# Kernel optimization log

Hardware: AMD Instinct MI355X
Metric: run time of the kernel (lower is better)

Reference implementation:

```python
import jax, jax.numpy as jnp
import numpy as np

B, H, W = 16, 1024, 1024
EPS = 1e-7
FG_PROB = 0.1  # foreground pixel probability for synthetic gt


def setup_inputs() -> dict:
    key = jax.random.key(0)
    k1, k2 = jax.random.split(key)
    probs = jax.random.normal(k1, (B, 2, H, W), dtype=jnp.float32)
    gt = (jax.random.uniform(k2, (B, H, W)) < FG_PROB).astype(jnp.float32)
    gt_f_num = gt.sum(axis=(1, 2))  # per-sample foreground pixel count (float)
    return {"probs": probs, "gt": gt, "gt_f_num": gt_f_num, "img_h": H, "img_w": W}


def reference(probs, gt, gt_f_num, img_h, img_w):
    # foreground probability, clamped
    pc = jax.nn.softmax(probs, axis=1)[:, 1, :, :]
    pc = jnp.clip(pc, EPS, 1.0 - EPS)
    b = pc.shape[0]
    f_loss = -(gt * jnp.log(pc)).reshape(b, -1)          # [B, N]
    b_loss = -((1.0 - gt) * jnp.log(1.0 - pc)).reshape(b, -1)  # [B, N]
    n = b_loss.shape[1]

    # sort background loss descending per sample; top gt_f_num[i] entries are
    # "difficult" negatives, the rest are "simple" (equivalent to the torch
    # gather-into-zero-buffers since only sums/counts are taken afterwards)
    sorted_b = -jnp.sort(-b_loss, axis=1)                # descending, [B, N]
    k = gt_f_num.astype(jnp.int32)                       # int(gt_f_num[i])
    mask = jnp.arange(n, dtype=jnp.int32)[None, :] < k[:, None]  # [B, N]

    difficult_sum = jnp.sum(jnp.where(mask, sorted_b, 0.0), axis=1)
    simple_sum = jnp.sum(jnp.where(mask, 0.0, sorted_b), axis=1)
    difficult_num = jnp.sum(mask & (sorted_b != 0.0), axis=1).astype(jnp.float32)

    difficult_b_loss = difficult_sum / (difficult_num + 1e-16)
    simple_b_loss = simple_sum / (float(img_h * img_w) + 1e-16)
    f_loss_mean = f_loss.sum(axis=1) / (gt_f_num + 1e-16)

    return difficult_b_loss.mean() + f_loss_mean.mean() + simple_b_loss.mean()
```

## Files before the change

kernel.cpp:

```cpp
#include <hip/hip_runtime.h>
#include <math.h>

#define NB 16
#define NPIX 1048576
#define BINS 4096
#define CHUNKS 64
#define TPB_A 512
#define PIX_PER_BLOCK (NPIX / CHUNKS)
#define PPT 8
#define ITERS_A (PIX_PER_BLOCK / (TPB_A * PPT))
#define TPB_B 256
#define BINS_PER_CHUNK (BINS / TPB_B)
#define BLOSS_MAX 16.2f
#define BINW (BLOSS_MAX / (float)BINS)
#define B_CAP 15.9424f
#define F_CAP 16.1181f

__device__ __forceinline__ void fadd_glb(float* p, float v) {
    __hip_atomic_fetch_add(p, v, __ATOMIC_RELAXED, __HIP_MEMORY_SCOPE_AGENT);
}

__global__ __launch_bounds__(TPB_A) void pass_a(
    const float* __restrict__ probs, const float* __restrict__ gt,
    unsigned* __restrict__ g_cnt, float* __restrict__ f_sum,
    float* __restrict__ b_sum)
{
    __shared__ unsigned s_cnt[BINS];
    __shared__ float s_redf[TPB_A / 64];
    __shared__ float s_redb[TPB_A / 64];

    const int tid = threadIdx.x;
    for (int j = tid; j < BINS; j += TPB_A) s_cnt[j] = 0u;
    __syncthreads();

    const int blk = blockIdx.x;
    const int b = blk / CHUNKS;
    const int chunk = blk % CHUNKS;
    const float* p0 = probs + (size_t)b * 2 * NPIX;
    const float* p1 = p0 + NPIX;
    const float* gp = gt + (size_t)b * NPIX;
    const int base = chunk * PIX_PER_BLOCK;
    const float scale = (float)BINS / BLOSS_MAX;

    float f_acc = 0.f, b_acc = 0.f;

    float4 cA0, cB0, cA1, cB1, cG0, cG1;
    {
        const int i = base + (tid << 2);
        const int i2 = i + TPB_A * 4;
        cA0 = *(const float4*)(p0 + i);  cB0 = *(const float4*)(p0 + i2);
        cA1 = *(const float4*)(p1 + i);  cB1 = *(const float4*)(p1 + i2);
        cG0 = *(const float4*)(gp + i);  cG1 = *(const float4*)(gp + i2);
    }
    for (int it = 0; it < ITERS_A; ++it) {
        float4 nA0, nB0, nA1, nB1, nG0, nG1;
        {
            const int nit = (it + 1 < ITERS_A) ? it + 1 : it;
            const int i = base + nit * (TPB_A * PPT) + (tid << 2);
            const int i2 = i + TPB_A * 4;
            nA0 = *(const float4*)(p0 + i);  nB0 = *(const float4*)(p0 + i2);
            nA1 = *(const float4*)(p1 + i);  nB1 = *(const float4*)(p1 + i2);
            nG0 = *(const float4*)(gp + i);  nG1 = *(const float4*)(gp + i2);
        }
        const float dv[PPT] = {cA1.x - cA0.x, cA1.y - cA0.y, cA1.z - cA0.z, cA1.w - cA0.w,
                               cB1.x - cB0.x, cB1.y - cB0.y, cB1.z - cB0.z, cB1.w - cB0.w};
        const float gv[PPT] = {cG0.x, cG0.y, cG0.z, cG0.w, cG1.x, cG1.y, cG1.z, cG1.w};
        #pragma unroll
        for (int q = 0; q < PPT; ++q) {
            const float d = dv[q];
            const float sp = fmaxf(d, 0.f) + __logf(1.f + __expf(-fabsf(d)));
            if (gv[q] > 0.5f) {
                f_acc += fminf(sp - d, F_CAP);
            } else {
                const float bl = fminf(sp, B_CAP);
                b_acc += bl;
                int bin = (int)(bl * scale);
                bin = bin < (BINS - 1) ? bin : (BINS - 1);
                atomicAdd(&s_cnt[bin], 1u);
            }
        }
        cA0 = nA0; cB0 = nB0; cA1 = nA1; cB1 = nB1; cG0 = nG0; cG1 = nG1;
    }
    __syncthreads();

    for (int j = tid; j < BINS; j += TPB_A) {
        const unsigned c = s_cnt[j];
        if (c) atomicAdd(&g_cnt[(size_t)b * BINS + j], c);
    }

    #pragma unroll
    for (int o = 32; o > 0; o >>= 1) {
        f_acc += __shfl_down(f_acc, o, 64);
        b_acc += __shfl_down(b_acc, o, 64);
    }
    if ((tid & 63) == 0) { s_redf[tid >> 6] = f_acc; s_redb[tid >> 6] = b_acc; }
    __syncthreads();
    if (tid == 0) {
        float f = 0.f, bs = 0.f;
        #pragma unroll
        for (int w = 0; w < TPB_A / 64; ++w) { f += s_redf[w]; bs += s_redb[w]; }
        fadd_glb(&f_sum[b], f);
        fadd_glb(&b_sum[b], bs);
    }
}

__global__ __launch_bounds__(TPB_B) void pass_b(
    const unsigned* __restrict__ g_cnt, const float* __restrict__ f_sum,
    const float* __restrict__ b_sum, const float* __restrict__ gt_f_num,
    float* __restrict__ terms)
{
    __shared__ unsigned s_cnt[BINS];
    __shared__ unsigned s_suf[TPB_B];
    __shared__ double s_wsuf[TPB_B];
    __shared__ double s_dsum;

    const int b = blockIdx.x;
    const int t = threadIdx.x;

    for (int j = 0; j < BINS_PER_CHUNK; ++j) {
        const int bin = j * TPB_B + t;
        s_cnt[bin] = g_cnt[(size_t)b * BINS + bin];
    }
    __syncthreads();

    unsigned c = 0; double w = 0.0;
    const int cb = t * BINS_PER_CHUNK;
    for (int j = 0; j < BINS_PER_CHUNK; ++j) {
        const unsigned cc = s_cnt[cb + j];
        c += cc;
        w += (double)cc * (double)(((float)(cb + j) + 0.5f) * BINW);
    }
    s_suf[t] = c; s_wsuf[t] = w;
    __syncthreads();

    for (int off = 1; off < TPB_B; off <<= 1) {
        const unsigned ac = (t + off < TPB_B) ? s_suf[t + off] : 0u;
        const double aw = (t + off < TPB_B) ? s_wsuf[t + off] : 0.0;
        __syncthreads();
        s_suf[t] += ac; s_wsuf[t] += aw;
        __syncthreads();
    }

    const long long kk = (long long)gt_f_num[b];
    const unsigned long long n_pos = (unsigned long long)s_suf[0];
    const unsigned long long suf_me = s_suf[t];
    const unsigned long long suf_nx = (t + 1 < TPB_B) ? s_suf[t + 1] : 0ull;

    if (kk > 0 && (unsigned long long)kk < n_pos &&
        suf_nx < (unsigned long long)kk && (unsigned long long)kk <= suf_me) {
        unsigned long long cum = suf_nx;
        double W = (t + 1 < TPB_B) ? s_wsuf[t + 1] : 0.0;
        int bstar = cb;
        for (int j = BINS_PER_CHUNK - 1; j >= 0; --j) {
            const int bin = cb + j;
            const unsigned cc = s_cnt[bin];
            if (cum + cc >= (unsigned long long)kk) { bstar = bin; break; }
            cum += cc;
            W += (double)cc * (double)(((float)bin + 0.5f) * BINW);
        }
        const double partial = (double)(kk - (long long)cum);
        s_dsum = W + partial * (double)(((float)bstar + 0.5f) * BINW);
    }
    __syncthreads();

    if (t == 0) {
        const double S_total = (double)b_sum[b];
        const double fs = (double)f_sum[b];
        const double gfn = (double)gt_f_num[b];
        double dsum, dnum;
        if (kk <= 0) { dsum = 0.0; dnum = 0.0; }
        else if ((unsigned long long)kk >= n_pos) { dsum = S_total; dnum = (double)n_pos; }
        else { dsum = s_dsum; dnum = (double)kk; }
        const double term = dsum / (dnum + 1e-16)
                          + fs / (gfn + 1e-16)
                          + (S_total - dsum) / ((double)NPIX + 1e-16);
        terms[b] = (float)term;
    }
}

__global__ void pass_c(const float* __restrict__ terms, float* __restrict__ out)
{
    if (threadIdx.x == 0 && blockIdx.x == 0) {
        float s = 0.f;
        #pragma unroll
        for (int i = 0; i < NB; ++i) s += terms[i];
        out[0] = s / (float)NB;
    }
}

extern "C" void kernel_launch(void* const* d_in, const int* in_sizes, int n_in,
                              void* d_out, int out_size, void* d_ws, size_t ws_size,
                              hipStream_t stream) {
    const float* probs = (const float*)d_in[0];
    const float* gt    = (const float*)d_in[1];
    const float* gfn   = (const float*)d_in[2];
    char* ws = (char*)d_ws;

    const size_t hist_bytes = (size_t)NB * BINS * 4;
    unsigned* g_cnt = (unsigned*)ws;
    float*    f_sum = (float*)(ws + hist_bytes);
    float*    b_sum = f_sum + NB;
    float*    terms = b_sum + NB;

    hipMemsetAsync(ws, 0, hist_bytes + 2 * NB * sizeof(float), stream);

    hipLaunchKernelGGL(pass_a, dim3(NB * CHUNKS), dim3(TPB_A), 0, stream,
                       probs, gt, g_cnt, f_sum, b_sum);
    hipLaunchKernelGGL(pass_b, dim3(NB), dim3(TPB_B), 0, stream,
                       g_cnt, f_sum, b_sum, gfn, terms);
    hipLaunchKernelGGL(pass_c, dim3(1), dim3(64), 0, stream,
                       terms, (float*)d_out);
}
```

Baseline: 244.2 us.

## Use 1024-thread blocks, single-shot loads, replicated global histograms, fewer bins

The pass_a kernel now launches 1024 threads per block. Each thread loads all four of its float4 quads at once, so the software-pipelined loop is gone. The foreground/background accumulation is made branchless using the gt values as multipliers, and only the histogram atomic stays conditional. The histogram is cut to 2048 bins over a wider range with a raised background cap, and it is flushed into 8 replicated per-sample global copies to spread atomic contention. pass_b sums the replicas back together. The coarser bins and changed caps alter the approximation of the top-k background loss, which may affect accuracy.

```diff
diff --git a/kernel.cpp b/kernel.cpp
--- a/kernel.cpp
+++ b/kernel.cpp
@@ -3,24 +3,24 @@
 
 #define NB 16
 #define NPIX 1048576
-#define BINS 4096
+#define BINS 2048
 #define CHUNKS 64
-#define TPB_A 512
+#define TPB_A 1024
 #define PIX_PER_BLOCK (NPIX / CHUNKS)
-#define PPT 8
-#define ITERS_A (PIX_PER_BLOCK / (TPB_A * PPT))
+#define QUADS 4
+#define REPL 8
 #define TPB_B 256
 #define BINS_PER_CHUNK (BINS / TPB_B)
-#define BLOSS_MAX 16.2f
+#define BLOSS_MAX 16.7f
 #define BINW (BLOSS_MAX / (float)BINS)
-#define B_CAP 15.9424f
+#define B_CAP 16.636f
 #define F_CAP 16.1181f
 
 __device__ __forceinline__ void fadd_glb(float* p, float v) {
     __hip_atomic_fetch_add(p, v, __ATOMIC_RELAXED, __HIP_MEMORY_SCOPE_AGENT);
 }
 
-__global__ __launch_bounds__(TPB_A) void pass_a(
+__global__ __launch_bounds__(TPB_A, 8) void pass_a(
     const float* __restrict__ probs, const float* __restrict__ gt,
     unsigned* __restrict__ g_cnt, float* __restrict__ f_sum,
     float* __restrict__ b_sum)
@@ -30,7 +30,8 @@
     __shared__ float s_redb[TPB_A / 64];
 
     const int tid = threadIdx.x;
-    for (int j = tid; j < BINS; j += TPB_A) s_cnt[j] = 0u;
+    #pragma unroll
+    for (int j = 0; j < BINS / TPB_A; ++j) s_cnt[j * TPB_A + tid] = 0u;
     __syncthreads();
 
     const int blk = blockIdx.x;
@@ -42,50 +43,46 @@
     const int base = chunk * PIX_PER_BLOCK;
     const float scale = (float)BINS / BLOSS_MAX;
 
+    float4 A0[QUADS], A1[QUADS], G[QUADS];
+    #pragma unroll
+    for (int q = 0; q < QUADS; ++q) {
+        const int i = base + ((q * TPB_A + tid) << 2);
+        A0[q] = *(const float4*)(p0 + i);
+        A1[q] = *(const float4*)(p1 + i);
+        G[q]  = *(const float4*)(gp + i);
+    }
+
     float f_acc = 0.f, b_acc = 0.f;
-
-    float4 cA0, cB0, cA1, cB1, cG0, cG1;
-    {
-        const int i = base + (tid << 2);
-        const int i2 = i + TPB_A * 4;
-        cA0 = *(const float4*)(p0 + i);  cB0 = *(const float4*)(p0 + i2);
-        cA1 = *(const float4*)(p1 + i);  cB1 = *(const float4*)(p1 + i2);
-        cG0 = *(const float4*)(gp + i);  cG1 = *(const float4*)(gp + i2);
-    }
-    for (int it = 0; it < ITERS_A; ++it) {
-        float4 nA0, nB0, nA1, nB1, nG0, nG1;
-        {
-            const int nit = (it + 1 < ITERS_A) ? it + 1 : it;
-            const int i = base + nit * (TPB_A * PPT) + (tid << 2);
-            const int i2 = i + TPB_A * 4;
-            nA0 = *(const float4*)(p0 + i);  nB0 = *(const float4*)(p0 + i2);
-            nA1 = *(const float4*)(p1 + i);  nB1 = *(const float4*)(p1 + i2);
-            nG0 = *(const float4*)(gp + i);  nG1 = *(const float4*)(gp + i2);
-        }
-        const float dv[PPT] = {cA1.x - cA0.x, cA1.y - cA0.y, cA1.z - cA0.z, cA1.w - cA0.w,
-                               cB1.x - cB0.x, cB1.y - cB0.y, cB1.z - cB0.z, cB1.w - cB0.w};
-        const float gv[PPT] = {cG0.x, cG0.y, cG0.z, cG0.w, cG1.x, cG1.y, cG1.z, cG1.w};
-        #pragma unroll
-        for (int q = 0; q < PPT; ++q) {
-            const float d = dv[q];
+    #pragma unroll
+    for (int q = 0; q < QUADS; ++q) {
+        const float dv[4] = {A1[q].x - A0[q].x, A1[q].y - A0[q].y,
+                             A1[q].z - A0[q].z, A1[q].w - A0[q].w};
+        const float gv[4] = {G[q].x, G[q].y, G[q].z, G[q].w};
+        #pragma unroll
+        for (int c = 0; c < 4; ++c) {
+            const float d = dv[c];
+            const float g = gv[c];
             const float sp = fmaxf(d, 0.f) + __logf(1.f + __expf(-fabsf(d)));
-            if (gv[q] > 0.5f) {
-                f_acc += fminf(sp - d, F_CAP);
-            } else {
-                const float bl = fminf(sp, B_CAP);
-                b_acc += bl;
+            f_acc += g * fminf(sp - d, F_CAP);
+            const float bl = fminf(sp, B_CAP);
+            b_acc += (1.f - g) * bl;
+            if (g < 0.5f) {
                 int bin = (int)(bl * scale);
                 bin = bin < (BINS - 1) ? bin : (BINS - 1);
                 atomicAdd(&s_cnt[bin], 1u);
             }
         }
-        cA0 = nA0; cB0 = nB0; cA1 = nA1; cB1 = nB1; cG0 = nG0; cG1 = nG1;
-    }
-    __syncthreads();
-
-    for (int j = tid; j < BINS; j += TPB_A) {
-        const unsigned c = s_cnt[j];
-        if (c) atomicAdd(&g_cnt[(size_t)b * BINS + j], c);
+    }
+    __syncthreads();
+
+    {
+        unsigned* dst = g_cnt + ((size_t)b * REPL + (chunk & (REPL - 1))) * BINS;
+        #pragma unroll
+        for (int j = 0; j < BINS / TPB_A; ++j) {
+            const int bin = j * TPB_A + tid;
+            const unsigned c = s_cnt[bin];
+            if (c) atomicAdd(&dst[bin], c);
+        }
     }
 
     #pragma unroll
@@ -117,14 +114,20 @@
     const int b = blockIdx.x;
     const int t = threadIdx.x;
 
+    #pragma unroll
     for (int j = 0; j < BINS_PER_CHUNK; ++j) {
         const int bin = j * TPB_B + t;
-        s_cnt[bin] = g_cnt[(size_t)b * BINS + bin];
+        unsigned c = 0;
+        #pragma unroll
+        for (int r = 0; r < REPL; ++r)
+            c += g_cnt[((size_t)b * REPL + r) * BINS + bin];
+        s_cnt[bin] = c;
     }
     __syncthreads();
 
     unsigned c = 0; double w = 0.0;
     const int cb = t * BINS_PER_CHUNK;
+    #pragma unroll
     for (int j = 0; j < BINS_PER_CHUNK; ++j) {
         const unsigned cc = s_cnt[cb + j];
         c += cc;
@@ -196,7 +199,7 @@
     const float* gfn   = (const float*)d_in[2];
     char* ws = (char*)d_ws;
 
-    const size_t hist_bytes = (size_t)NB * BINS * 4;
+    const size_t hist_bytes = (size_t)NB * REPL * BINS * 4;
     unsigned* g_cnt = (unsigned*)ws;
     float*    f_sum = (float*)(ws + hist_bytes);
     float*    b_sum = f_sum + NB;
```

After: 250.7 us. 1.03x slower.
